# Performance work log

Hardware: AMD Instinct MI355X
Metric: run time of the kernel (lower is better)

The kernel has to match this reference:

```python
import jax, jax.numpy as jnp
import numpy as np
import math

DN = ('NCHW', 'OIHW', 'NCHW')
TOTAL_STRIDE = 8.0
SCORE_OFFSET = 3.0
SCORE_SIZE = 25
BN_EPS = 1e-5


def conv2d(x, w, b, pad):
    y = jax.lax.conv_general_dilated(x, w, (1, 1), [(pad, pad), (pad, pad)],
                                     dimension_numbers=DN)
    return y + b[None, :, None, None]


def conv_module(x, w1, b1, ws, bs):
    x = conv2d(x, w1, b1, 1)
    for i in range(ws.shape[0]):
        x = conv2d(jax.nn.relu(x), ws[i], bs[i], 1)
    return x


def bn_eval(x, g, b):
    # inference-mode BatchNorm2d: running_mean=0, running_var=1
    s = g / jnp.sqrt(1.0 + BN_EPS)
    return x * s[None, :, None, None] + b[None, :, None, None]


def memory_read(fm, fq):
    B, C, T, H, W = fm.shape
    fm_flat = fm.reshape(B, C, T * H * W)          # (B, C, THW)
    fq_flat = fq.reshape(B, C, H * W)              # (B, C, HW)
    # scores: (B, THW, HW), softmax over the memory axis (THW)
    w = jnp.einsum('bct,bcq->btq', fm_flat, fq_flat) / math.sqrt(512.0)
    w = jax.nn.softmax(w, axis=1)
    mem = jnp.einsum('bct,btq->bcq', fm_flat, w).reshape(B, C, H, W)
    return jnp.concatenate([mem, fq], axis=1)      # (B, 2C, H, W)


def fm_ctr():
    gx = SCORE_OFFSET + TOTAL_STRIDE * jnp.arange(SCORE_SIZE, dtype=jnp.float32)[None, :]
    gy = SCORE_OFFSET + TOTAL_STRIDE * jnp.arange(SCORE_SIZE, dtype=jnp.float32)[:, None]
    return jnp.stack([jnp.broadcast_to(gx, (SCORE_SIZE, SCORE_SIZE)),
                      jnp.broadcast_to(gy, (SCORE_SIZE, SCORE_SIZE))], axis=-1)  # (H,W,2)


def reference(fm, fq, cls1_w, cls1_b, clsk_w, clsk_b, reg1_w, reg1_b, regk_w, regk_b,
              w_cls, b_cls, g_cls, be_cls, w_ctr, b_ctr, g_ctr, be_ctr,
              w_off, b_off, g_off, be_off, si, bi):
    y = memory_read(fm, fq)
    cls_feat = conv_module(y, cls1_w, cls1_b, clsk_w, clsk_b)
    reg_feat = conv_module(y, reg1_w, reg1_b, regk_w, regk_b)
    cls_score = bn_eval(conv2d(cls_feat, w_cls, b_cls, 0), g_cls, be_cls)  # (B,1,H,W)
    ctr_score = bn_eval(conv2d(cls_feat, w_ctr, b_ctr, 0), g_ctr, be_ctr)  # (B,1,H,W)
    offsets = bn_eval(conv2d(reg_feat, w_off, b_off, 0), g_off, be_off)    # (B,4,H,W)

    B = cls_score.shape[0]
    cls_score = cls_score.transpose(0, 2, 3, 1).reshape(B, -1, 1)
    ctr_score = ctr_score.transpose(0, 2, 3, 1).reshape(B, -1, 1)
    offsets = jnp.exp(si * offsets + bi) * TOTAL_STRIDE

    ctr = fm_ctr()                                  # (H,W,2)
    off = offsets.transpose(0, 2, 3, 1)             # (B,H,W,4)
    xy0 = ctr[None] - off[..., :2]
    xy1 = ctr[None] + off[..., 2:]
    bbox = jnp.concatenate([xy0, xy1], axis=-1).reshape(B, -1, 4)
    return cls_score, ctr_score, bbox


def setup_inputs() -> dict:
    key = jax.random.key(0)
    ks = jax.random.split(key, 16)
    B, C, T, H, W = 8, 20, 24, 25, 25
    WSC = 0.02  # small conv-weight scale to keep the 7-conv stack + exp() stable
    inp = {
        'fm': jax.random.normal(ks[0], (B, C, T, H, W), jnp.float32),
        'fq': jax.random.normal(ks[1], (B, C, H, W), jnp.float32),
        'cls1_w': jax.random.normal(ks[2], (256, 40, 3, 3), jnp.float32) * WSC,
        'cls1_b': jnp.zeros((256,), jnp.float32),
        'clsk_w': jax.random.normal(ks[3], (6, 256, 256, 3, 3), jnp.float32) * WSC,
        'clsk_b': jnp.zeros((6, 256), jnp.float32),
        'reg1_w': jax.random.normal(ks[4], (256, 40, 3, 3), jnp.float32) * WSC,
        'reg1_b': jnp.zeros((256,), jnp.float32),
        'regk_w': jax.random.normal(ks[5], (6, 256, 256, 3, 3), jnp.float32) * WSC,
        'regk_b': jnp.zeros((6, 256), jnp.float32),
        'w_cls': jax.random.normal(ks[6], (1, 256, 1, 1), jnp.float32) * WSC,
        'b_cls': jnp.zeros((1,), jnp.float32),
        'g_cls': jnp.ones((1,), jnp.float32),
        'be_cls': jnp.zeros((1,), jnp.float32),
        'w_ctr': jax.random.normal(ks[7], (1, 256, 1, 1), jnp.float32) * WSC,
        'b_ctr': jnp.zeros((1,), jnp.float32),
        'g_ctr': jnp.ones((1,), jnp.float32),
        'be_ctr': jnp.zeros((1,), jnp.float32),
        'w_off': jax.random.normal(ks[8], (4, 256, 1, 1), jnp.float32) * WSC,
        'b_off': jnp.zeros((4,), jnp.float32),
        'g_off': jnp.ones((4,), jnp.float32),
        'be_off': jnp.zeros((4,), jnp.float32),
        'si': jnp.float32(1.0),
        'bi': jnp.float32(0.0),
    }
    return inp
```

## Files before the change

### kernel.cpp

```cpp
#include <hip/hip_runtime.h>
#include <math.h>

#define BATCH 8
#define CCH 20
#define THW 15000
#define HW 625
#define SSIDE 25
#define PHW 729

#define NKEY 15000
#define TPAD 15104
#define NKT 118
#define NKC 20
#define KCHUNK 6

typedef __attribute__((ext_vector_type(8))) short bf16x8;
typedef __attribute__((ext_vector_type(4))) float f32x4;

#define YBF_OFF  0ULL
#define XA_OFF   746496ULL
#define XB_OFF   6718464ULL
#define WT0_OFF  12690432ULL
#define WT_OFF   13280256ULL
#define WTL_ELEMS 1179648ULL
#define FMT_OFF  27436032ULL
#define FM32_OFF 35169280ULL
#define FQB_OFF  42902528ULL
#define PART_OFF 43230208ULL

__device__ __forceinline__ ushort f2bf(float x) {
    unsigned u = __float_as_uint(x);
    u = (u + 0x7FFFu + ((u >> 16) & 1u)) >> 16;
    return (ushort)u;
}
__device__ __forceinline__ float bf2f(ushort v) {
    return __uint_as_float(((unsigned)v) << 16);
}

__device__ __forceinline__ void gload16(const void* g, void* l) {
    __builtin_amdgcn_global_load_lds((const __attribute__((address_space(1))) void*)g,
                                     (__attribute__((address_space(3))) void*)l, 16, 0, 0);
}

__global__ __launch_bounds__(256) void prep_fm(const float* __restrict__ fm,
                                               ushort* __restrict__ fmbT,
                                               ushort* __restrict__ fmb32) {
    __shared__ ushort sT2[256][34];
    const int tid = threadIdx.x;
    const int t0 = blockIdx.x * 256;
    const int b = blockIdx.y;
    const int t = t0 + tid;
    #pragma unroll 4
    for (int c = 0; c < CCH; c++) {
        float v = (t < NKEY) ? fm[((size_t)b * CCH + c) * THW + t] : 0.f;
        ushort h = f2bf(v);
        sT2[tid][c] = h;
        fmb32[((size_t)b * 32 + c) * TPAD + t] = h;
    }
    #pragma unroll
    for (int cz = CCH; cz < 32; cz++)
        fmb32[((size_t)b * 32 + cz) * TPAD + t] = 0;
    __syncthreads();
    const int g = tid >> 4, j = tid & 15;
    uint* dstb = (uint*)fmbT + ((size_t)b * TPAD + t0) * 16 + j;
    #pragma unroll
    for (int i = 0; i < 16; i++) {
        int r = g + 16 * i;
        uint v = 0;
        if (j < 10) v = *(const uint*)&sT2[r][2 * j];
        dstb[(size_t)r * 16] = v;
    }
}

__global__ __launch_bounds__(256) void prep_fq(const float* __restrict__ fq,
                                               ushort* __restrict__ fqb) {
    int idx = blockIdx.x * 256 + threadIdx.x;
    if (idx >= BATCH * 640) return;
    int b = idx / 640, q = idx % 640;
    const float qscale = 1.4426950408889634f * 0.04419417382415922f;
    ushort* dst = fqb + (size_t)idx * 32;
    #pragma unroll 4
    for (int c = 0; c < CCH; c++) {
        float v = (q < HW) ? fq[((size_t)b * CCH + c) * HW + q] * qscale : 0.f;
        dst[c] = f2bf(v);
    }
    #pragma unroll
    for (int c = CCH; c < 32; c++) dst[c] = 0;
}

__global__ __launch_bounds__(512) void attn_flash(const ushort* __restrict__ fmbT,
                                                  const ushort* __restrict__ fmb32,
                                                  const ushort* __restrict__ fqb,
                                                  char* __restrict__ part) {
    __shared__ __align__(16) ushort sK[2][4096];
    __shared__ __align__(16) ushort sV[2][4096];
    __shared__ __align__(16) ushort sP[8][2048];
    const int tid = threadIdx.x;
    const int wave = tid >> 6, lane = tid & 63;
    const int q16 = lane & 15, quad = lane >> 4;
    const int phys = blockIdx.x;
    const int lid = (phys & 7) * 60 + (phys >> 3);
    const int b = lid / 60;
    const int rem = lid - b * 60;
    const int kc = rem / 3;
    const int xq = rem - kc * 3;
    const int qt0 = xq * 2 + (wave >> 2);
    const bool act = (qt0 < 5);
    const int qt = act ? qt0 : 4;
    const int wq = wave & 3;

    bf16x8 Qf[2];
    #pragma unroll
    for (int nf = 0; nf < 2; nf++)
        Qf[nf] = *(const bf16x8*)(fqb + ((size_t)(b * 640 + qt * 128 + wq * 32 + nf * 16 + q16) << 5) + quad * 8);

    f32x4 O[2][2];
    #pragma unroll
    for (int nf = 0; nf < 2; nf++) { O[nf][0] = (f32x4)0.f; O[nf][1] = (f32x4)0.f; }
    float lp0 = 0.f, lp1 = 0.f;
    const f32x4 zz = (f32x4)0.f;

    const int kt0 = kc * KCHUNK;
    const int kt1 = (kt0 + KCHUNK < NKT) ? kt0 + KCHUNK : NKT;

    const int rK = tid >> 2, cK = tid & 3;
    const int rV = tid >> 4, cV = tid & 15;
    const ushort* srcK = fmbT + ((size_t)(b * TPAD + rK) << 5) + ((cK ^ (rK & 3)) << 3);
    const ushort* srcV = fmb32 + (size_t)(b * 32 + rV) * TPAD + ((cV ^ (rV & 7)) << 3);
    auto stage = [&](int kt, int bufi) {
        const int t0s = kt << 7;
        gload16(srcK + ((size_t)t0s << 5), &sK[bufi][wave << 9]);
        gload16(srcV + t0s, &sV[bufi][wave << 9]);
    };

    const int q3 = q16 & 3, q7 = q16 & 7;
    uint* const pBase = (uint*)&sP[wave][q16 << 7];

    int buf = 0;
    stage(kt0, 0);
    for (int kt = kt0; kt < kt1; kt++) {
        if (kt + 1 < kt1) {
            stage(kt + 1, buf ^ 1);
            asm volatile("s_waitcnt vmcnt(2)\n\ts_barrier" ::: "memory");
        } else {
            asm volatile("s_waitcnt vmcnt(0)\n\ts_barrier" ::: "memory");
        }
        const int t0 = kt << 7;
        const bool tail = (t0 + 128 > NKEY);

        bf16x8 Ak[8], Av[8];
        #pragma unroll
        for (int m = 0; m < 8; m++)
            Ak[m] = *(const bf16x8*)&sK[buf][((m * 16 + q16) << 5) + ((quad ^ q3) << 3)];
        #pragma unroll
        for (int mp = 0; mp < 4; mp++)
            #pragma unroll
            for (int cf = 0; cf < 2; cf++)
                Av[mp * 2 + cf] = *(const bf16x8*)&sV[buf][((cf * 16 + q16) << 7) + (((mp * 4 + quad) ^ q7) << 3)];

        f32x4 S[8][2];
        #pragma unroll
        for (int m = 0; m < 8; m++) {
            S[m][0] = __builtin_amdgcn_mfma_f32_16x16x32_bf16(Ak[m], Qf[0], zz, 0, 0, 0);
            S[m][1] = __builtin_amdgcn_mfma_f32_16x16x32_bf16(Ak[m], Qf[1], zz, 0, 0, 0);
        }

        #pragma unroll
        for (int nf = 0; nf < 2; nf++) {
            float lacc = 0.f;
            #pragma unroll
            for (int m = 0; m < 8; m++) {
                float p[4];
                #pragma unroll
                for (int i = 0; i < 4; i++) {
                    float v = __builtin_amdgcn_exp2f(S[m][nf][i]);
                    if (tail && (t0 + m * 16 + quad * 4 + i >= NKEY)) v = 0.f;
                    p[i] = v;
                }
                lacc += (p[0] + p[1]) + (p[2] + p[3]);
                uint pk0 = __builtin_amdgcn_perm(__float_as_uint(p[1]) + 0x8000u,
                                                 __float_as_uint(p[0]) + 0x8000u, 0x07060302u);
                uint pk1 = __builtin_amdgcn_perm(__float_as_uint(p[3]) + 0x8000u,
                                                 __float_as_uint(p[2]) + 0x8000u, 0x07060302u);
                uint* dst = pBase + (((m ^ q7) << 3) + quad * 2);
                dst[0] = pk0;
                dst[1] = pk1;
            }
            if (nf == 0) lp0 += lacc; else lp1 += lacc;
            #pragma unroll
            for (int mp = 0; mp < 4; mp++) {
                bf16x8 Bp = *(const bf16x8*)(pBase + ((mp * 16 + quad * 4) ^ (q7 << 3)));
                O[nf][0] = __builtin_amdgcn_mfma_f32_16x16x32_bf16(Av[mp * 2 + 0], Bp, O[nf][0], 0, 0, 0);
                O[nf][1] = __builtin_amdgcn_mfma_f32_16x16x32_bf16(Av[mp * 2 + 1], Bp, O[nf][1], 0, 0, 0);
            }
        }
        asm volatile("s_waitcnt lgkmcnt(0)\n\ts_barrier" ::: "memory");
        buf ^= 1;
    }

    lp0 += __shfl_xor(lp0, 16); lp0 += __shfl_xor(lp0, 32);
    lp1 += __shfl_xor(lp1, 16); lp1 += __shfl_xor(lp1, 32);

    if (act) {
        #pragma unroll
        for (int nf = 0; nf < 2; nf++) {
            int ql = wq * 32 + nf * 16 + q16;
            size_t rec = ((((size_t)b * 5 + qt) * NKC + kc) * 128 + ql) * 48;
            uint2 pk;
            pk.x = (unsigned)f2bf(O[nf][0][0]) | ((unsigned)f2bf(O[nf][0][1]) << 16);
            pk.y = (unsigned)f2bf(O[nf][0][2]) | ((unsigned)f2bf(O[nf][0][3]) << 16);
            *(uint2*)(part + rec + quad * 8) = pk;
            if (quad == 0) {
                uint2 pk1;
                pk1.x = (unsigned)f2bf(O[nf][1][0]) | ((unsigned)f2bf(O[nf][1][1]) << 16);
                pk1.y = (unsigned)f2bf(O[nf][1][2]) | ((unsigned)f2bf(O[nf][1][3]) << 16);
                *(uint2*)(part + rec + 32) = pk1;
                *(float*)(part + rec + 40) = (nf == 0) ? lp0 : lp1;
            }
        }
    }
}

__device__ __forceinline__ int border_pp(int bi) {
    if (bi < 27) return bi;
    if (bi < 54) return 26 * 27 + (bi - 27);
    if (bi < 79) return (bi - 53) * 27;
    return (bi - 78) * 27 + 26;
}
__global__ __launch_bounds__(256) void attn_merge_zero(const char* __restrict__ part,
                                                       const float* __restrict__ fq,
                                                       ushort* __restrict__ ybf,
                                                       ushort* __restrict__ xa,
                                                       ushort* __restrict__ xb) {
    if (blockIdx.x < 20) {
        int g = blockIdx.x * 256 + threadIdx.x;
        if (g >= BATCH * HW) return;
        int b = g / HW, q = g % HW;
        int qt = q >> 7, ql = q & 127;
        const char* pb = part + ((((size_t)b * 5 + qt) * NKC) * 128 + ql) * 48;
        float L = 0.f;
        float acc[CCH];
        #pragma unroll
        for (int c = 0; c < CCH; c++) acc[c] = 0.f;
        for (int kc = 0; kc < NKC; kc++) {
            const char* rec = pb + (size_t)kc * 128 * 48;
            L += *(const float*)(rec + 40);
            const ushort* av = (const ushort*)rec;
            #pragma unroll
            for (int c = 0; c < CCH; c++) acc[c] += bf2f(av[c]);
        }
        float inv = 1.f / L;
        int pp = (q / 25 + 1) * 27 + (q % 25) + 1;
        ushort* yb = ybf + ((size_t)b * PHW + pp) * 64;
        #pragma unroll
        for (int c = 0; c < CCH; c++) yb[c] = f2bf(acc[c] * inv);
        #pragma unroll
        for (int c = 0; c < CCH; c++) yb[20 + c] = f2bf(fq[((size_t)b * CCH + c) * HW + q]);
        #pragma unroll
        for (int c = 40; c < 64; c++) yb[c] = 0;
    } else {
        int idx = (blockIdx.x - 20) * 256 + threadIdx.x;
        ushort* buf; int cin;
        if (idx < 6656) { buf = ybf; cin = 64; }
        else if (idx < 59904) { idx -= 6656; buf = xa; cin = 256; }
        else if (idx < 113152) { idx -= 59904; buf = xb; cin = 256; }
        else return;
        int nc = cin >> 3;
        int per = 104 * nc;
        int img = idx / per, r = idx - img * per;
        int bi = r / nc, cc = r - bi * nc;
        int pp = border_pp(bi);
        uint4 z = make_uint4(0, 0, 0, 0);
        *(uint4*)&buf[((size_t)img * PHW + pp) * cin + cc * 8] = z;
    }
}

__global__ __launch_bounds__(256) void prep_weights(const float* __restrict__ cw1,
                                                    const float* __restrict__ rw1,
                                                    const float* __restrict__ cwk,
                                                    const float* __restrict__ rwk,
                                                    ushort* __restrict__ wt0,
                                                    ushort* __restrict__ wt) {
    int bid = blockIdx.x;
    if (bid < 1152) {
        int idx = bid * 256 + threadIdx.x;
        if (idx >= 2 * 9 * 256 * 64) return;
        int ic = idx & 63;
        int oc = (idx >> 6) & 255;
        int t = idx >> 14;
        int kyx = t % 9;
        int br = t / 9;
        float v = 0.f;
        if (ic < 40) {
            const float* w = br ? rw1 : cw1;
            v = w[((size_t)oc * 40 + ic) * 9 + kyx];
        }
        wt0[idx] = f2bf(v);
    } else {
        int rb = bid - 1152;
        int s = rb >> 9;
        int idx = (rb & 511) * 256 + threadIdx.x;
        if (idx >= 2 * 256 * 256) return;
        int ic = idx & 255;
        int oc = (idx >> 8) & 255;
        int br = idx >> 16;
        const float* w = br ? rwk : cwk;
        const float* src = w + (((size_t)s * 256 + oc) * 256 + ic) * 9;
        ushort* dst = wt + (size_t)s * WTL_ELEMS;
        float v[9];
        #pragma unroll
        for (int k = 0; k < 9; k++) v[k] = src[k];
        #pragma unroll
        for (int k = 0; k < 9; k++)
            dst[(((size_t)(br * 9 + k)) * 256 + oc) * 256 + ic] = f2bf(v[k]);
    }
}

__global__ __launch_bounds__(256) void conv_gemm(
    const ushort* __restrict__ xin, int cin, int cshift, int in_shared, int relu_out,
    const ushort* __restrict__ wt, const float* __restrict__ bias_c,
    const float* __restrict__ bias_r, ushort* __restrict__ xout) {
    __shared__ __align__(16) ushort sA[2][4096];
    __shared__ __align__(16) ushort sB[2][4096];
    const int tid = threadIdx.x;
    const int lane = tid & 63;
    const int wave = tid >> 6;
    const int n16 = lane & 15, quad = lane >> 4;
    const int wm = wave & 1, wn = wave >> 1;
    const int phys = blockIdx.x;
    const int lid = (phys & 7) * 80 + (phys >> 3);
    const int bb = lid / 40;
    const int rr2 = lid - bb * 40;
    const int ot = rr2 & 3, nt = rr2 >> 2;
    const int oc0 = ot * 64;
    const ushort* wbr = wt + (size_t)(bb < 8 ? 0 : 1) * 9 * 256 * cin;
    const float* bias = (bb < 8) ? bias_c : bias_r;
    const ushort* inb = xin + (size_t)(in_shared ? (bb & 7) : bb) * PHW * cin;

    const int l8 = lane >> 3, j8 = lane & 7;
    const int r0 = wave * 16 + l8;
    const int jj = j8 ^ (l8 & 7);
    const int segA = wave * 1024;

    const ushort* aS0 = wbr + (size_t)(oc0 + r0) * cin + jj * 8;
    const ushort* aS1 = aS0 + (size_t)8 * cin;
    const int p0 = nt * 64 + r0;
    const int p1 = p0 + 8;
    const int pe0 = (p0 < HW) ? p0 : (HW - 1);
    const int pe1 = (p1 < HW) ? p1 : (HW - 1);
    const ushort* bS0 = inb + (size_t)((pe0 / 25) * 27 + (pe0 % 25)) * cin + jj * 8;
    const ushort* bS1 = inb + (size_t)((pe1 / 25) * 27 + (pe1 % 25)) * cin + jj * 8;

    const int NIT = 9 << cshift;
    const int cmask = (1 << cshift) - 1;

    auto issue = [&](int it, int buf) {
        const int kyx = it >> cshift;
        const int ccc = it & cmask;
        const int ky = (kyx >= 6) ? 2 : (kyx >= 3 ? 1 : 0);
        const int kx = kyx - ky * 3;
        const int aoff = kyx * 256 * cin + ccc * 64;
        const int boff = (ky * 27 + kx) * cin + ccc * 64;
        gload16(aS0 + aoff, &sA[buf][segA]);
        gload16(aS1 + aoff, &sA[buf][segA + 512]);
        gload16(bS0 + boff, &sB[buf][segA]);
        gload16(bS1 + boff, &sB[buf][segA + 512]);
    };

    f32x4 acc00 = (f32x4)0.f, acc01 = (f32x4)0.f;
    f32x4 acc10 = (f32x4)0.f, acc11 = (f32x4)0.f;
    const int arow0 = wm * 32 + n16;
    const int brow0 = wn * 32 + n16;
    const int h8 = n16 & 7;

    auto mfma_tile = [&](const ushort* sa, const ushort* sb) {
        #pragma unroll
        for (int ks = 0; ks < 2; ks++) {
            const int swz = ((ks * 4 + quad) ^ h8) * 8;
            bf16x8 a0 = *(const bf16x8*)&sa[arow0 * 64 + swz];
            bf16x8 a1 = *(const bf16x8*)&sa[(arow0 + 16) * 64 + swz];
            bf16x8 b0 = *(const bf16x8*)&sb[brow0 * 64 + swz];
            bf16x8 b1 = *(const bf16x8*)&sb[(brow0 + 16) * 64 + swz];
            acc00 = __builtin_amdgcn_mfma_f32_16x16x32_bf16(a0, b0, acc00, 0, 0, 0);
            acc01 = __builtin_amdgcn_mfma_f32_16x16x32_bf16(a0, b1, acc01, 0, 0, 0);
            acc10 = __builtin_amdgcn_mfma_f32_16x16x32_bf16(a1, b0, acc10, 0, 0, 0);
            acc11 = __builtin_amdgcn_mfma_f32_16x16x32_bf16(a1, b1, acc11, 0, 0, 0);
        }
    };

    issue(0, 0);
    asm volatile("s_waitcnt vmcnt(0)\n\ts_barrier" ::: "memory");

    for (int it = 0; it < NIT; it++) {
        if (it + 1 < NIT) issue(it + 1, (it + 1) & 1);
        mfma_tile(sA[it & 1], sB[it & 1]);
        asm volatile("s_waitcnt vmcnt(0) lgkmcnt(0)\n\ts_barrier" ::: "memory");
    }

    f32x4 accs[2][2] = {{acc00, acc01}, {acc10, acc11}};
    #pragma unroll
    for (int mf = 0; mf < 2; mf++) {
        int ocb = oc0 + wm * 32 + mf * 16 + quad * 4;
        float4 bv = *(const float4*)(bias + ocb);
        #pragma unroll
        for (int nf = 0; nf < 2; nf++) {
            int pcol = nt * 64 + wn * 32 + nf * 16 + n16;
            if (pcol >= HW) continue;
            int pp = (pcol / 25 + 1) * 27 + (pcol % 25) + 1;
            f32x4 a = accs[mf][nf];
            float v0 = a[0] + bv.x;
            float v1 = a[1] + bv.y;
            float v2 = a[2] + bv.z;
            float v3 = a[3] + bv.w;
            if (relu_out) {
                v0 = fmaxf(v0, 0.f); v1 = fmaxf(v1, 0.f);
                v2 = fmaxf(v2, 0.f); v3 = fmaxf(v3, 0.f);
            }
            uint2 st;
            st.x = (unsigned)f2bf(v0) | ((unsigned)f2bf(v1) << 16);
            st.y = (unsigned)f2bf(v2) | ((unsigned)f2bf(v3) << 16);
            *(uint2*)(&xout[((size_t)bb * PHW + pp) * 256 + ocb]) = st;
        }
    }
}

__global__ __launch_bounds__(256) void heads(const ushort* __restrict__ X,
                                             const float* __restrict__ wcls, const float* __restrict__ bcls,
                                             const float* __restrict__ gcls, const float* __restrict__ becls,
                                             const float* __restrict__ wctr, const float* __restrict__ bctr,
                                             const float* __restrict__ gctr, const float* __restrict__ bectr,
                                             const float* __restrict__ woff, const float* __restrict__ boff,
                                             const float* __restrict__ goff, const float* __restrict__ beoff,
                                             const float* __restrict__ si, const float* __restrict__ bi,
                                             float* __restrict__ out) {
    int g = blockIdx.x * 256 + threadIdx.x;
    if (g >= BATCH * HW) return;
    int b = g / HW, p = g % HW;
    int pp = (p / 25 + 1) * 27 + (p % 25) + 1;
    const ushort* fc = X + ((size_t)b * PHW + pp) * 256;
    const ushort* fr = X + ((size_t)(8 + b) * PHW + pp) * 256;
    float ac = 0.f, at = 0.f, a0 = 0.f, a1 = 0.f, a2 = 0.f, a3 = 0.f;
    for (int c0 = 0; c0 < 256; c0 += 8) {
        uint4 vc = *(const uint4*)(fc + c0);
        uint4 vr = *(const uint4*)(fr + c0);
        unsigned wc_[4] = {vc.x, vc.y, vc.z, vc.w};
        unsigned wr_[4] = {vr.x, vr.y, vr.z, vr.w};
        #pragma unroll
        for (int j = 0; j < 4; j++) {
            float cl = __uint_as_float(wc_[j] << 16);
            float ch = __uint_as_float(wc_[j] & 0xFFFF0000u);
            float rl = __uint_as_float(wr_[j] << 16);
            float rh = __uint_as_float(wr_[j] & 0xFFFF0000u);
            int c = c0 + j * 2;
            ac += wcls[c] * cl + wcls[c + 1] * ch;
            at += wctr[c] * cl + wctr[c + 1] * ch;
            a0 += woff[c] * rl + woff[c + 1] * rh;
            a1 += woff[256 + c] * rl + woff[256 + c + 1] * rh;
            a2 += woff[512 + c] * rl + woff[512 + c + 1] * rh;
            a3 += woff[768 + c] * rl + woff[768 + c + 1] * rh;
        }
    }
    const float bns = 1.f / sqrtf(1.f + 1e-5f);
    float cls = (ac + bcls[0]) * (gcls[0] * bns) + becls[0];
    float ctr = (at + bctr[0]) * (gctr[0] * bns) + bectr[0];
    float sv = si[0], bv = bi[0];
    float o0 = (a0 + boff[0]) * (goff[0] * bns) + beoff[0];
    float o1 = (a1 + boff[1]) * (goff[1] * bns) + beoff[1];
    float o2 = (a2 + boff[2]) * (goff[2] * bns) + beoff[2];
    float o3 = (a3 + boff[3]) * (goff[3] * bns) + beoff[3];
    float e0 = __expf(sv * o0 + bv) * 8.f;
    float e1 = __expf(sv * o1 + bv) * 8.f;
    float e2 = __expf(sv * o2 + bv) * 8.f;
    float e3 = __expf(sv * o3 + bv) * 8.f;
    float gx = 3.f + 8.f * (float)(p % SSIDE);
    float gy = 3.f + 8.f * (float)(p / SSIDE);
    out[g] = cls;
    out[BATCH * HW + g] = ctr;
    float* bbx = out + 2 * BATCH * HW + (size_t)g * 4;
    bbx[0] = gx - e0;
    bbx[1] = gy - e1;
    bbx[2] = gx + e2;
    bbx[3] = gy + e3;
}

extern "C" void kernel_launch(void* const* d_in, const int* in_sizes, int n_in,
                              void* d_out, int out_size, void* d_ws, size_t ws_size,
                              hipStream_t stream) {
    const float* fm     = (const float*)d_in[0];
    const float* fq     = (const float*)d_in[1];
    const float* cls1_w = (const float*)d_in[2];
    const float* cls1_b = (const float*)d_in[3];
    const float* clsk_w = (const float*)d_in[4];
    const float* clsk_b = (const float*)d_in[5];
    const float* reg1_w = (const float*)d_in[6];
    const float* reg1_b = (const float*)d_in[7];
    const float* regk_w = (const float*)d_in[8];
    const float* regk_b = (const float*)d_in[9];
    const float* w_cls  = (const float*)d_in[10];
    const float* b_cls  = (const float*)d_in[11];
    const float* g_cls  = (const float*)d_in[12];
    const float* be_cls = (const float*)d_in[13];
    const float* w_ctr  = (const float*)d_in[14];
    const float* b_ctr  = (const float*)d_in[15];
    const float* g_ctr  = (const float*)d_in[16];
    const float* be_ctr = (const float*)d_in[17];
    const float* w_off  = (const float*)d_in[18];
    const float* b_off  = (const float*)d_in[19];
    const float* g_off  = (const float*)d_in[20];
    const float* be_off = (const float*)d_in[21];
    const float* si     = (const float*)d_in[22];
    const float* bi     = (const float*)d_in[23];

    char* ws = (char*)d_ws;
    ushort* YBF  = (ushort*)(ws + YBF_OFF);
    ushort* XA   = (ushort*)(ws + XA_OFF);
    ushort* XB   = (ushort*)(ws + XB_OFF);
    ushort* WT0  = (ushort*)(ws + WT0_OFF);
    ushort* WT   = (ushort*)(ws + WT_OFF);
    ushort* FMT  = (ushort*)(ws + FMT_OFF);
    ushort* FM32 = (ushort*)(ws + FM32_OFF);
    ushort* FQB  = (ushort*)(ws + FQB_OFF);
    char*   PART = ws + PART_OFF;

    prep_fm<<<dim3(59, 8), 256, 0, stream>>>(fm, FMT, FM32);
    prep_fq<<<dim3(20), 256, 0, stream>>>(fq, FQB);
    attn_flash<<<dim3(480), 512, 0, stream>>>(FMT, FM32, FQB, PART);
    attn_merge_zero<<<dim3(462), 256, 0, stream>>>(PART, fq, YBF, XA, XB);

    prep_weights<<<dim3(1152 + 512 * 6), 256, 0, stream>>>(cls1_w, reg1_w, clsk_w, regk_w, WT0, WT);

    conv_gemm<<<dim3(640), 256, 0, stream>>>(YBF, 64, 0, 1, 1, WT0, cls1_b, reg1_b, XA);

    ushort* cur = XA;
    ushort* nxt = XB;
    for (int s = 0; s < 6; s++) {
        int relu_out = (s < 5) ? 1 : 0;
        conv_gemm<<<dim3(640), 256, 0, stream>>>(cur, 256, 2, 0, relu_out,
            WT + (size_t)s * WTL_ELEMS,
            clsk_b + (size_t)s * 256, regk_b + (size_t)s * 256, nxt);
        ushort* tmp = cur; cur = nxt; nxt = tmp;
    }

    heads<<<dim3(20), 256, 0, stream>>>(cur, w_cls, b_cls, g_cls, be_cls,
                                        w_ctr, b_ctr, g_ctr, be_ctr,
                                        w_off, b_off, g_off, be_off, si, bi,
                                        (float*)d_out);
}
```

Measured before the change: 365.5 us.

## Reuse a padded input halo tile across all nine conv taps in shared memory

The implicit-GEMM conv kernel used to reload a 64-position by 64-channel input tile from global memory for every one of the nine 3x3 taps. It now loads one contiguous halo strip of 128 padded rows per channel chunk into a larger double-buffered shared tile. Each tap then reads from that strip at a row shift, with a per-row XOR swizzle, and the strip for the next chunk is prefetched during the first four taps. This cuts global B traffic roughly ninefold, at the cost of twice the B shared memory and more complex wait logic. Separately, the heads kernel now splits the 256 channels across four quads with shuffle reductions, so it launches 79 blocks instead of 20.

```diff
diff --git a/kernel.cpp b/kernel.cpp
--- a/kernel.cpp
+++ b/kernel.cpp
@@ -317,11 +317,11 @@
 }
 
 __global__ __launch_bounds__(256) void conv_gemm(
-    const ushort* __restrict__ xin, int cin, int cshift, int in_shared, int relu_out,
+    const ushort* __restrict__ xin, int cin, int in_shared, int relu_out,
     const ushort* __restrict__ wt, const float* __restrict__ bias_c,
     const float* __restrict__ bias_r, ushort* __restrict__ xout) {
     __shared__ __align__(16) ushort sA[2][4096];
-    __shared__ __align__(16) ushort sB[2][4096];
+    __shared__ __align__(16) ushort sBh[2][8192];
     const int tid = threadIdx.x;
     const int lane = tid & 63;
     const int wave = tid >> 6;
@@ -338,49 +338,48 @@
     const ushort* inb = xin + (size_t)(in_shared ? (bb & 7) : bb) * PHW * cin;
 
     const int l8 = lane >> 3, j8 = lane & 7;
-    const int r0 = wave * 16 + l8;
-    const int jj = j8 ^ (l8 & 7);
+    const int jj = j8 ^ l8;
+
+    const int rA = wave * 16 + l8;
+    const ushort* aS0 = wbr + (size_t)(oc0 + rA) * cin + jj * 8;
+    const ushort* aS1 = aS0 + (size_t)8 * cin;
     const int segA = wave * 1024;
 
-    const ushort* aS0 = wbr + (size_t)(oc0 + r0) * cin + jj * 8;
-    const ushort* aS1 = aS0 + (size_t)8 * cin;
-    const int p0 = nt * 64 + r0;
-    const int p1 = p0 + 8;
-    const int pe0 = (p0 < HW) ? p0 : (HW - 1);
-    const int pe1 = (p1 < HW) ? p1 : (HW - 1);
-    const ushort* bS0 = inb + (size_t)((pe0 / 25) * 27 + (pe0 % 25)) * cin + jj * 8;
-    const ushort* bS1 = inb + (size_t)((pe1 / 25) * 27 + (pe1 % 25)) * cin + jj * 8;
-
-    const int NIT = 9 << cshift;
-    const int cmask = (1 << cshift) - 1;
-
-    auto issue = [&](int it, int buf) {
-        const int kyx = it >> cshift;
-        const int ccc = it & cmask;
-        const int ky = (kyx >= 6) ? 2 : (kyx >= 3 ? 1 : 0);
-        const int kx = kyx - ky * 3;
-        const int aoff = kyx * 256 * cin + ccc * 64;
-        const int boff = (ky * 27 + kx) * cin + ccc * 64;
+    const int p0 = nt * 64;
+    const int ppb = p0 + 2 * (p0 / 25);
+    const ushort* bS = inb + (size_t)ppb * cin + jj * 8;
+
+    const int NCH = cin >> 6;
+
+    auto issueA = [&](int ch, int kyx, int buf) {
+        const int aoff = kyx * 256 * cin + ch * 64;
         gload16(aS0 + aoff, &sA[buf][segA]);
         gload16(aS1 + aoff, &sA[buf][segA + 512]);
-        gload16(bS0 + boff, &sB[buf][segA]);
-        gload16(bS1 + boff, &sB[buf][segA + 512]);
+    };
+    auto issueB1 = [&](int ch, int q, int buf) {
+        const int rb = (wave * 4 + q) * 8;
+        gload16(bS + (size_t)(rb + l8) * cin + ch * 64, &sBh[buf][rb * 64]);
     };
 
     f32x4 acc00 = (f32x4)0.f, acc01 = (f32x4)0.f;
     f32x4 acc10 = (f32x4)0.f, acc11 = (f32x4)0.f;
     const int arow0 = wm * 32 + n16;
-    const int brow0 = wn * 32 + n16;
     const int h8 = n16 & 7;
-
-    auto mfma_tile = [&](const ushort* sa, const ushort* sb) {
+    const int pos0 = p0 + wn * 32 + n16;
+    const int pos1 = pos0 + 16;
+    const int PR0 = pos0 + 28 + 2 * (pos0 / 25) - ppb;
+    const int PR1 = pos1 + 28 + 2 * (pos1 / 25) - ppb;
+
+    auto mfma_tap = [&](const ushort* sa, const ushort* sbh, int d) {
+        const int row0 = PR0 + d, row1 = PR1 + d;
+        const int m0 = row0 & 7, m1 = row1 & 7;
         #pragma unroll
         for (int ks = 0; ks < 2; ks++) {
-            const int swz = ((ks * 4 + quad) ^ h8) * 8;
-            bf16x8 a0 = *(const bf16x8*)&sa[arow0 * 64 + swz];
-            bf16x8 a1 = *(const bf16x8*)&sa[(arow0 + 16) * 64 + swz];
-            bf16x8 b0 = *(const bf16x8*)&sb[brow0 * 64 + swz];
-            bf16x8 b1 = *(const bf16x8*)&sb[(brow0 + 16) * 64 + swz];
+            const int cq = ks * 4 + quad;
+            bf16x8 a0 = *(const bf16x8*)&sa[arow0 * 64 + ((cq ^ h8) << 3)];
+            bf16x8 a1 = *(const bf16x8*)&sa[(arow0 + 16) * 64 + ((cq ^ h8) << 3)];
+            bf16x8 b0 = *(const bf16x8*)&sbh[row0 * 64 + ((cq ^ m0) << 3)];
+            bf16x8 b1 = *(const bf16x8*)&sbh[row1 * 64 + ((cq ^ m1) << 3)];
             acc00 = __builtin_amdgcn_mfma_f32_16x16x32_bf16(a0, b0, acc00, 0, 0, 0);
             acc01 = __builtin_amdgcn_mfma_f32_16x16x32_bf16(a0, b1, acc01, 0, 0, 0);
             acc10 = __builtin_amdgcn_mfma_f32_16x16x32_bf16(a1, b0, acc10, 0, 0, 0);
@@ -388,13 +387,26 @@
         }
     };
 
-    issue(0, 0);
+    issueB1(0, 0, 0); issueB1(0, 1, 0); issueB1(0, 2, 0); issueB1(0, 3, 0);
+    issueA(0, 0, 0);
     asm volatile("s_waitcnt vmcnt(0)\n\ts_barrier" ::: "memory");
 
-    for (int it = 0; it < NIT; it++) {
-        if (it + 1 < NIT) issue(it + 1, (it + 1) & 1);
-        mfma_tile(sA[it & 1], sB[it & 1]);
-        asm volatile("s_waitcnt vmcnt(0) lgkmcnt(0)\n\ts_barrier" ::: "memory");
+    int itg = 0;
+    for (int c = 0; c < NCH; c++) {
+        #pragma unroll
+        for (int kyx = 0; kyx < 9; kyx++, itg++) {
+            if (itg + 1 < NCH * 9) {
+                const int nk = (kyx == 8) ? 0 : kyx + 1;
+                const int nc = (kyx == 8) ? c + 1 : c;
+                issueA(nc, nk, (itg + 1) & 1);
+            }
+            const bool bpf = (kyx < 4) && (c + 1 < NCH);
+            if (bpf) issueB1(c + 1, kyx, (c + 1) & 1);
+            const int ky = kyx / 3, kx = kyx % 3;
+            mfma_tap(sA[itg & 1], sBh[c & 1], (ky - 1) * 27 + (kx - 1));
+            if (bpf) asm volatile("s_waitcnt vmcnt(1)\n\ts_barrier" ::: "memory");
+            else     asm volatile("s_waitcnt vmcnt(0)\n\ts_barrier" ::: "memory");
+        }
     }
 
     f32x4 accs[2][2] = {{acc00, acc01}, {acc10, acc11}};
@@ -433,14 +445,19 @@
                                              const float* __restrict__ goff, const float* __restrict__ beoff,
                                              const float* __restrict__ si, const float* __restrict__ bi,
                                              float* __restrict__ out) {
-    int g = blockIdx.x * 256 + threadIdx.x;
-    if (g >= BATCH * HW) return;
-    int b = g / HW, p = g % HW;
-    int pp = (p / 25 + 1) * 27 + (p % 25) + 1;
-    const ushort* fc = X + ((size_t)b * PHW + pp) * 256;
-    const ushort* fr = X + ((size_t)(8 + b) * PHW + pp) * 256;
+    const int lane = threadIdx.x & 63, wave = threadIdx.x >> 6;
+    const int gw = blockIdx.x * 4 + wave;
+    const int g = gw * 16 + (lane & 15);
+    const int quad = lane >> 4;
+    const bool valid = (g < BATCH * HW);
+    const int gc = valid ? g : (BATCH * HW - 1);
+    const int b = gc / HW, p = gc % HW;
+    const int pp = (p / 25 + 1) * 27 + (p % 25) + 1;
+    const ushort* fc = X + ((size_t)b * PHW + pp) * 256 + quad * 64;
+    const ushort* fr = X + ((size_t)(8 + b) * PHW + pp) * 256 + quad * 64;
     float ac = 0.f, at = 0.f, a0 = 0.f, a1 = 0.f, a2 = 0.f, a3 = 0.f;
-    for (int c0 = 0; c0 < 256; c0 += 8) {
+    #pragma unroll
+    for (int c0 = 0; c0 < 64; c0 += 8) {
         uint4 vc = *(const uint4*)(fc + c0);
         uint4 vr = *(const uint4*)(fr + c0);
         unsigned wc_[4] = {vc.x, vc.y, vc.z, vc.w};
@@ -451,7 +468,7 @@
             float ch = __uint_as_float(wc_[j] & 0xFFFF0000u);
             float rl = __uint_as_float(wr_[j] << 16);
             float rh = __uint_as_float(wr_[j] & 0xFFFF0000u);
-            int c = c0 + j * 2;
+            int c = quad * 64 + c0 + j * 2;
             ac += wcls[c] * cl + wcls[c + 1] * ch;
             at += wctr[c] * cl + wctr[c + 1] * ch;
             a0 += woff[c] * rl + woff[c + 1] * rh;
@@ -460,27 +477,35 @@
             a3 += woff[768 + c] * rl + woff[768 + c + 1] * rh;
         }
     }
-    const float bns = 1.f / sqrtf(1.f + 1e-5f);
-    float cls = (ac + bcls[0]) * (gcls[0] * bns) + becls[0];
-    float ctr = (at + bctr[0]) * (gctr[0] * bns) + bectr[0];
-    float sv = si[0], bv = bi[0];
-    float o0 = (a0 + boff[0]) * (goff[0] * bns) + beoff[0];
-    float o1 = (a1 + boff[1]) * (goff[1] * bns) + beoff[1];
-    float o2 = (a2 + boff[2]) * (goff[2] * bns) + beoff[2];
-    float o3 = (a3 + boff[3]) * (goff[3] * bns) + beoff[3];
-    float e0 = __expf(sv * o0 + bv) * 8.f;
-    float e1 = __expf(sv * o1 + bv) * 8.f;
-    float e2 = __expf(sv * o2 + bv) * 8.f;
-    float e3 = __expf(sv * o3 + bv) * 8.f;
-    float gx = 3.f + 8.f * (float)(p % SSIDE);
-    float gy = 3.f + 8.f * (float)(p / SSIDE);
-    out[g] = cls;
-    out[BATCH * HW + g] = ctr;
-    float* bbx = out + 2 * BATCH * HW + (size_t)g * 4;
-    bbx[0] = gx - e0;
-    bbx[1] = gy - e1;
-    bbx[2] = gx + e2;
-    bbx[3] = gy + e3;
+    ac += __shfl_xor(ac, 16); at += __shfl_xor(at, 16);
+    a0 += __shfl_xor(a0, 16); a1 += __shfl_xor(a1, 16);
+    a2 += __shfl_xor(a2, 16); a3 += __shfl_xor(a3, 16);
+    ac += __shfl_xor(ac, 32); at += __shfl_xor(at, 32);
+    a0 += __shfl_xor(a0, 32); a1 += __shfl_xor(a1, 32);
+    a2 += __shfl_xor(a2, 32); a3 += __shfl_xor(a3, 32);
+    if (quad == 0 && valid) {
+        const float bns = 1.f / sqrtf(1.f + 1e-5f);
+        float cls = (ac + bcls[0]) * (gcls[0] * bns) + becls[0];
+        float ctr = (at + bctr[0]) * (gctr[0] * bns) + bectr[0];
+        float sv = si[0], bv = bi[0];
+        float o0 = (a0 + boff[0]) * (goff[0] * bns) + beoff[0];
+        float o1 = (a1 + boff[1]) * (goff[1] * bns) + beoff[1];
+        float o2 = (a2 + boff[2]) * (goff[2] * bns) + beoff[2];
+        float o3 = (a3 + boff[3]) * (goff[3] * bns) + beoff[3];
+        float e0 = __expf(sv * o0 + bv) * 8.f;
+        float e1 = __expf(sv * o1 + bv) * 8.f;
+        float e2 = __expf(sv * o2 + bv) * 8.f;
+        float e3 = __expf(sv * o3 + bv) * 8.f;
+        float gx = 3.f + 8.f * (float)(p % SSIDE);
+        float gy = 3.f + 8.f * (float)(p / SSIDE);
+        out[g] = cls;
+        out[BATCH * HW + g] = ctr;
+        float* bbx = out + 2 * BATCH * HW + (size_t)g * 4;
+        bbx[0] = gx - e0;
+        bbx[1] = gy - e1;
+        bbx[2] = gx + e2;
+        bbx[3] = gy + e3;
+    }
 }
 
 extern "C" void kernel_launch(void* const* d_in, const int* in_sizes, int n_in,
@@ -529,19 +554,19 @@
 
     prep_weights<<<dim3(1152 + 512 * 6), 256, 0, stream>>>(cls1_w, reg1_w, clsk_w, regk_w, WT0, WT);
 
-    conv_gemm<<<dim3(640), 256, 0, stream>>>(YBF, 64, 0, 1, 1, WT0, cls1_b, reg1_b, XA);
+    conv_gemm<<<dim3(640), 256, 0, stream>>>(YBF, 64, 1, 1, WT0, cls1_b, reg1_b, XA);
 
     ushort* cur = XA;
     ushort* nxt = XB;
     for (int s = 0; s < 6; s++) {
         int relu_out = (s < 5) ? 1 : 0;
-        conv_gemm<<<dim3(640), 256, 0, stream>>>(cur, 256, 2, 0, relu_out,
+        conv_gemm<<<dim3(640), 256, 0, stream>>>(cur, 256, 0, relu_out,
             WT + (size_t)s * WTL_ELEMS,
             clsk_b + (size_t)s * 256, regk_b + (size_t)s * 256, nxt);
         ushort* tmp = cur; cur = nxt; nxt = tmp;
     }
 
-    heads<<<dim3(20), 256, 0, stream>>>(cur, w_cls, b_cls, g_cls, be_cls,
+    heads<<<dim3(79), 256, 0, stream>>>(cur, w_cls, b_cls, g_cls, be_cls,
                                         w_ctr, b_ctr, g_ctr, be_ctr,
                                         w_off, b_off, g_off, be_off, si, bi,
                                         (float*)d_out);
```

After: 346.9 us. 5.1% less time.
